# Performance work log

Measured on AMD Instinct MI355X. Metric: run time of the kernel, lower is better.

Reference implementation:

```python
import jax, jax.numpy as jnp
import numpy as np

N_NODES = 100000
LN_EPS = 1e-5
NEG_SLOPE = 0.2


def setup_inputs() -> dict:
    key = jax.random.key(0)
    ks = jax.random.split(key, 6)
    N, E, NIN, EDIM, NOUT, H = N_NODES, 1600000, 64, 32, 128, 4
    x = jax.random.normal(ks[0], (N, NIN), dtype=jnp.float32)
    edge_index = jax.random.randint(ks[1], (2, E), 0, N, dtype=jnp.int64)
    edge_attr = jax.random.normal(ks[2], (E, EDIM), dtype=jnp.float32)
    # xavier-uniform linear weights (torch layout: [out, in])
    def xavier(k, fan_out, fan_in):
        lim = float(np.sqrt(6.0 / (fan_in + fan_out)))
        return jax.random.uniform(k, (fan_out, fan_in), jnp.float32, -lim, lim)
    W_msg = xavier(ks[3], NOUT, NIN + EDIM)          # (128, 96)
    W_att = xavier(ks[4], H, 2 * NIN + EDIM)         # (4, 160)
    bias = jnp.zeros((NOUT,), jnp.float32)
    ln_gamma = jnp.ones((NOUT,), jnp.float32)
    ln_beta = jnp.zeros((NOUT,), jnp.float32)
    return {"x": x, "edge_index": edge_index, "edge_attr": edge_attr,
            "W_msg": W_msg, "W_att": W_att, "bias": bias,
            "ln_gamma": ln_gamma, "ln_beta": ln_beta}


def reference(x, edge_index, edge_attr, W_msg, W_att, bias, ln_gamma, ln_beta):
    N = x.shape[0]
    H = W_att.shape[0]
    src, dst = edge_index[0], edge_index[1]
    xs = x[src]                                       # (E, node_in) gather
    xd = x[dst]                                       # (E, node_in) gather
    # message: W_msg @ [h_u ; x_uv]
    msg_in = jnp.concatenate([xs, edge_attr], axis=-1)            # (E, 96)
    msgs = msg_in @ W_msg.T                                        # (E, out_dim)
    msgs = msgs.reshape(-1, H, W_msg.shape[0] // H)                # (E, H, D)
    # attention logits: LeakyReLU(W_att @ [h_u ; h_v ; x_uv])
    att_in = jnp.concatenate([xs, xd, edge_attr], axis=-1)         # (E, 160)
    logits = att_in @ W_att.T                                      # (E, H)
    logits = jax.nn.leaky_relu(logits, NEG_SLOPE)
    # per-destination-node sparse softmax
    seg_max = jax.ops.segment_max(logits, dst, num_segments=N)     # (N, H)
    exp_l = jnp.exp(logits - seg_max[dst])                         # (E, H)
    seg_sum = jax.ops.segment_sum(exp_l, dst, num_segments=N)      # (N, H)
    att = exp_l / (seg_sum[dst] + 1e-9)                            # (E, H)
    # weighted scatter-add aggregation
    weighted = msgs * att[..., None]                               # (E, H, D)
    out = jax.ops.segment_sum(weighted, dst, num_segments=N)       # (N, H, D)
    out = out.reshape(N, -1) + bias                                # concat heads
    # layer norm over feature dim
    mu = out.mean(axis=-1, keepdims=True)
    var = out.var(axis=-1, keepdims=True)
    out = (out - mu) * jax.lax.rsqrt(var + LN_EPS) * ln_gamma + ln_beta
    return out
```

## Files before the change

kernel.cpp:

```cpp
#include <hip/hip_runtime.h>
#include <hip/hip_bf16.h>

typedef __attribute__((ext_vector_type(8))) short short8;
typedef __attribute__((ext_vector_type(4))) float f32x4;

__device__ __forceinline__ unsigned short fbf(float f) {
  union { float f; unsigned u; } v; v.f = f;
  unsigned r = v.u + 0x7fffu + ((v.u >> 16) & 1u);
  return (unsigned short)(r >> 16);
}
__device__ __forceinline__ unsigned pk2(float a, float b) {
  return (unsigned)fbf(a) | ((unsigned)fbf(b) << 16);
}
__device__ __forceinline__ float ubf(unsigned hi) {
  union { unsigned u; float f; } v; v.u = hi << 16; return v.f;
}
__device__ __forceinline__ float ubf_lo(unsigned u) {
  union { unsigned u; float f; } v; v.u = u << 16; return v.f;
}
__device__ __forceinline__ float ubf_hi(unsigned u) {
  union { unsigned u; float f; } v; v.u = u & 0xffff0000u; return v.f;
}
__device__ __forceinline__ float dot4(float4 a, float4 b) {
  return fmaf(a.x, b.x, fmaf(a.y, b.y, fmaf(a.z, b.z, a.w * b.w)));
}

__launch_bounds__(256)
__global__ void k_phase1(const float* __restrict__ x, const float* __restrict__ W_att,
                         const int* __restrict__ edst, int E,
                         float4* __restrict__ A_s, float4* __restrict__ A_d,
                         unsigned* __restrict__ xb32, int* __restrict__ deg,
                         int* __restrict__ rank, int N) {
  __shared__ float4 s_wa[160];
  if (threadIdx.x < 160) s_wa[threadIdx.x] = ((const float4*)W_att)[threadIdx.x];
  for (int i = blockIdx.x * blockDim.x + threadIdx.x; i < E; i += gridDim.x * blockDim.x)
    rank[i] = atomicAdd(&deg[edst[i]], 1);
  __syncthreads();
  for (int v = blockIdx.x * blockDim.x + threadIdx.x; v < N; v += gridDim.x * blockDim.x) {
    const float4* xp = (const float4*)&x[v * 64];
    float4 xq[16];
    #pragma unroll
    for (int k = 0; k < 16; k++) xq[k] = xp[k];
    float as[4] = {}, ad[4] = {};
    #pragma unroll
    for (int h = 0; h < 4; h++) {
      #pragma unroll
      for (int k = 0; k < 16; k++) {
        as[h] += dot4(s_wa[h * 40 + k], xq[k]);
        ad[h] += dot4(s_wa[h * 40 + 16 + k], xq[k]);
      }
    }
    A_s[v] = make_float4(as[0], as[1], as[2], as[3]);
    A_d[v] = make_float4(ad[0], ad[1], ad[2], ad[3]);
    #pragma unroll
    for (int k = 0; k < 16; k++) {
      xb32[v * 32 + 2 * k]     = pk2(xq[k].x, xq[k].y);
      xb32[v * 32 + 2 * k + 1] = pk2(xq[k].z, xq[k].w);
    }
  }
}

__global__ void k_scan1(const int* __restrict__ deg, int N, int* __restrict__ part,
                        int* __restrict__ bsum) {
  __shared__ int tmp[1024];
  int tid = threadIdx.x;
  int i = blockIdx.x * 1024 + tid;
  int dv = (i < N) ? deg[i] : 0;
  int v = (dv + 7) & ~7;
  tmp[tid] = v;
  __syncthreads();
  for (int ofs = 1; ofs < 1024; ofs <<= 1) {
    int t = (tid >= ofs) ? tmp[tid - ofs] : 0;
    __syncthreads();
    tmp[tid] += t;
    __syncthreads();
  }
  if (i < N) part[i] = tmp[tid] - v;
  if (tid == 1023) bsum[blockIdx.x] = tmp[tid];
}

__global__ void k_scan2(int* __restrict__ part, const int* __restrict__ bsum,
                        const int* __restrict__ deg, int N, int4* __restrict__ csrp) {
  __shared__ int sbase;
  if (threadIdx.x == 0) {
    int b = 0;
    for (int j = 0; j < (int)blockIdx.x; j++) b += bsum[j];
    sbase = b;
  }
  __syncthreads();
  int i = blockIdx.x * 1024 + threadIdx.x;
  if (i < N) {
    const int o = part[i] + sbase;
    part[i] = o;
    const int d = deg[i];
    const int pe = o + ((d + 7) & ~7);
    const int4 z = make_int4(0, 0, 0, 0);
    for (int s = o + d; s < pe; s++) csrp[s] = z;
    if (i == N - 1) part[N] = pe;
  }
}

__launch_bounds__(256)
__global__ void k_att2(const int* __restrict__ esrc, const int* __restrict__ edst, int E,
                       const float* __restrict__ ea, const float4* __restrict__ A_s,
                       const float4* __restrict__ A_d, const float* __restrict__ W_att,
                       uint2* __restrict__ att_eo, unsigned short* __restrict__ eab) {
  __shared__ float4 s_we[32];
  if (threadIdx.x < 32) {
    int h = threadIdx.x >> 3, k4 = threadIdx.x & 7;
    const float* p = &W_att[h * 160 + 128 + k4 * 4];
    s_we[threadIdx.x] = make_float4(p[0], p[1], p[2], p[3]);
  }
  __syncthreads();
  for (int e = blockIdx.x * blockDim.x + threadIdx.x; e < E; e += gridDim.x * blockDim.x) {
    const int s = esrc[e], d = edst[e];
    const float4* ep = (const float4*)&ea[(unsigned)e * 32u];
    float4 eq[8];
    #pragma unroll
    for (int k = 0; k < 8; k++) eq[k] = ep[k];
    if (eab) {
      uint4* eo = (uint4*)(eab + (size_t)e * 32u);
      uint4 u;
      u.x = pk2(eq[0].x, eq[0].y); u.y = pk2(eq[0].z, eq[0].w);
      u.z = pk2(eq[1].x, eq[1].y); u.w = pk2(eq[1].z, eq[1].w);
      eo[0] = u;
      u.x = pk2(eq[2].x, eq[2].y); u.y = pk2(eq[2].z, eq[2].w);
      u.z = pk2(eq[3].x, eq[3].y); u.w = pk2(eq[3].z, eq[3].w);
      eo[1] = u;
      u.x = pk2(eq[4].x, eq[4].y); u.y = pk2(eq[4].z, eq[4].w);
      u.z = pk2(eq[5].x, eq[5].y); u.w = pk2(eq[5].z, eq[5].w);
      eo[2] = u;
      u.x = pk2(eq[6].x, eq[6].y); u.y = pk2(eq[6].z, eq[6].w);
      u.z = pk2(eq[7].x, eq[7].y); u.w = pk2(eq[7].z, eq[7].w);
      eo[3] = u;
    }
    const float4 as4 = A_s[s], ad4 = A_d[d];
    const float base[4] = {as4.x + ad4.x, as4.y + ad4.y, as4.z + ad4.z, as4.w + ad4.w};
    float av[4];
    #pragma unroll
    for (int h = 0; h < 4; h++) {
      float lg = base[h];
      #pragma unroll
      for (int k = 0; k < 8; k++) lg += dot4(s_we[h * 8 + k], eq[k]);
      lg = fmaxf(lg, 0.2f * lg);
      av[h] = __expf(lg);
    }
    att_eo[e] = make_uint2(pk2(av[0], av[1]), pk2(av[2], av[3]));
  }
}

__launch_bounds__(256)
__global__ void k_scat(const int* __restrict__ esrc, const int* __restrict__ edst,
                       const int* __restrict__ rank, const int* __restrict__ offsets,
                       const uint2* __restrict__ att_eo, int E, int4* __restrict__ csrp) {
  for (int e = blockIdx.x * blockDim.x + threadIdx.x; e < E; e += gridDim.x * blockDim.x) {
    const int d = edst[e];
    const int slot = offsets[d] + rank[e];
    const uint2 a = att_eo[e];
    csrp[slot] = make_int4(esrc[e], e, (int)a.x, (int)a.y);
  }
}

__launch_bounds__(256)
__global__ void k_aggP(const unsigned short* __restrict__ xb, const float* __restrict__ ea,
                       const int4* __restrict__ csrp, const int* __restrict__ offsets,
                       unsigned short* __restrict__ agg, float* __restrict__ denom, int N) {
  __shared__ int4 s_ids[4][2][32];
  const int lane = threadIdx.x & 63;
  const int wvb = threadIdx.x >> 6;
  const int wv = (blockIdx.x * blockDim.x + threadIdx.x) >> 6;
  const int nw = (gridDim.x * blockDim.x) >> 6;
  const int l32 = lane & 31;
  const bool hi = lane >= 32;

  if (wv >= N) return;
  int v0 = wv;
  int sstart = __builtin_amdgcn_readfirstlane(offsets[v0]);
  int send   = __builtin_amdgcn_readfirstlane(offsets[v0 + 1]);
  int4 pre = csrp[sstart + l32];
  int buf = 0;

  while (true) {
    const int ng = (send - sstart) >> 3;
    const int nq = (ng + 3) >> 2;
    const int vn = v0 + nw;
    const int vc = (vn < N) ? vn : (N - 1);
    const int sstart_n = __builtin_amdgcn_readfirstlane(offsets[vc]);
    const int send_n   = __builtin_amdgcn_readfirstlane(offsets[vc + 1]);

    float ax0 = 0, ax1 = 0, ax2 = 0, ax3 = 0;
    float ae0 = 0, ae1 = 0, ae2 = 0, ae3 = 0;
    float dn0 = 0, dn1 = 0, dn2 = 0, dn3 = 0;

    for (int q = 0; q < nq; q++) {
      if (lane < 32) s_ids[wvb][buf][l32] = pre;
      const int nbase = (q + 1 < nq) ? (sstart + (q + 1) * 32) : sstart_n;
      pre = csrp[nbase + l32];
      const int nsc = min(4, ng - q * 4);
      float ev[4][8];
      unsigned short qv[4][8];
      #pragma unroll
      for (int sc = 0; sc < 4; sc++) {
        if (sc < nsc) {
          #pragma unroll
          for (int p = 0; p < 8; p++) {
            const int4 t_ = s_ids[wvb][buf][sc * 8 + p];
            qv[sc][p] = xb[(unsigned)(t_.x << 6) + lane];
            ev[sc][p] = ea[(unsigned)(t_.y << 5) + l32];
          }
        }
      }
      #pragma unroll
      for (int sc = 0; sc < 4; sc++) {
        if (sc < nsc) {
          #pragma unroll
          for (int p = 0; p < 8; p++) {
            const int4 t_ = s_ids[wvb][buf][sc * 8 + p];
            const float a0_ = ubf_lo((unsigned)t_.z);
            const float a1_ = ubf_hi((unsigned)t_.z);
            const float a2_ = ubf_lo((unsigned)t_.w);
            const float a3_ = ubf_hi((unsigned)t_.w);
            const float xf = ubf((unsigned)qv[sc][p]);
            const float evp = ev[sc][p];
            ax0 = fmaf(a0_, xf, ax0); ax1 = fmaf(a1_, xf, ax1);
            ax2 = fmaf(a2_, xf, ax2); ax3 = fmaf(a3_, xf, ax3);
            ae0 = fmaf(a0_, evp, ae0); ae1 = fmaf(a1_, evp, ae1);
            ae2 = fmaf(a2_, evp, ae2); ae3 = fmaf(a3_, evp, ae3);
            dn0 += a0_; dn1 += a1_; dn2 += a2_; dn3 += a3_;
          }
        }
      }
      buf ^= 1;
    }
    if (nq == 0) pre = csrp[sstart_n + l32];

    const unsigned base = (unsigned)v0 * 384u;
    agg[base + lane]        = fbf(ax0);
    agg[base + 96 + lane]   = fbf(ax1);
    agg[base + 192 + lane]  = fbf(ax2);
    agg[base + 288 + lane]  = fbf(ax3);
    const int hA = hi ? 2 : 0;
    agg[base + hA * 96 + 64 + l32]       = fbf(hi ? ae2 : ae0);
    agg[base + (hA + 1) * 96 + 64 + l32] = fbf(hi ? ae3 : ae1);
    if (lane == 0) ((float4*)denom)[v0] = make_float4(dn0, dn1, dn2, dn3);

    if (vn >= N) break;
    v0 = vn; sstart = sstart_n; send = send_n;
  }
}

__launch_bounds__(256)
__global__ void k_aggPb(const unsigned short* __restrict__ xb,
                        const unsigned short* __restrict__ eab,
                        const int4* __restrict__ csrp, const int* __restrict__ offsets,
                        unsigned short* __restrict__ agg, float* __restrict__ denom, int N) {
  __shared__ int4 s_ids[4][2][32];
  const int lane = threadIdx.x & 63;
  const int wvb = threadIdx.x >> 6;
  const int wv = (blockIdx.x * blockDim.x + threadIdx.x) >> 6;
  const int nw = (gridDim.x * blockDim.x) >> 6;
  const int l32 = lane & 31;
  const bool hi = lane >= 32;

  if (wv >= N) return;
  int v0 = wv;
  int sstart = __builtin_amdgcn_readfirstlane(offsets[v0]);
  int send   = __builtin_amdgcn_readfirstlane(offsets[v0 + 1]);
  int4 pre = csrp[sstart + l32];
  int buf = 0;

  while (true) {
    const int ng = (send - sstart) >> 3;
    const int nq = (ng + 3) >> 2;
    const int vn = v0 + nw;
    const int vc = (vn < N) ? vn : (N - 1);
    const int sstart_n = __builtin_amdgcn_readfirstlane(offsets[vc]);
    const int send_n   = __builtin_amdgcn_readfirstlane(offsets[vc + 1]);

    float ax0 = 0, ax1 = 0, ax2 = 0, ax3 = 0;
    float ae0 = 0, ae1 = 0, ae2 = 0, ae3 = 0;
    float dn0 = 0, dn1 = 0, dn2 = 0, dn3 = 0;

    for (int q = 0; q < nq; q++) {
      if (lane < 32) s_ids[wvb][buf][l32] = pre;
      const int nbase = (q + 1 < nq) ? (sstart + (q + 1) * 32) : sstart_n;
      pre = csrp[nbase + l32];
      const int nsc = min(4, ng - q * 4);
      unsigned short evb[4][8];
      unsigned short qv[4][8];
      #pragma unroll
      for (int sc = 0; sc < 4; sc++) {
        if (sc < nsc) {
          #pragma unroll
          for (int p = 0; p < 8; p++) {
            const int4 t_ = s_ids[wvb][buf][sc * 8 + p];
            qv[sc][p] = xb[(unsigned)(t_.x << 6) + lane];
            evb[sc][p] = eab[(unsigned)(t_.y << 5) + l32];
          }
        }
      }
      #pragma unroll
      for (int sc = 0; sc < 4; sc++) {
        if (sc < nsc) {
          #pragma unroll
          for (int p = 0; p < 8; p++) {
            const int4 t_ = s_ids[wvb][buf][sc * 8 + p];
            const float a0_ = ubf_lo((unsigned)t_.z);
            const float a1_ = ubf_hi((unsigned)t_.z);
            const float a2_ = ubf_lo((unsigned)t_.w);
            const float a3_ = ubf_hi((unsigned)t_.w);
            const float xf = ubf((unsigned)qv[sc][p]);
            const float evp = ubf((unsigned)evb[sc][p]);
            ax0 = fmaf(a0_, xf, ax0); ax1 = fmaf(a1_, xf, ax1);
            ax2 = fmaf(a2_, xf, ax2); ax3 = fmaf(a3_, xf, ax3);
            ae0 = fmaf(a0_, evp, ae0); ae1 = fmaf(a1_, evp, ae1);
            ae2 = fmaf(a2_, evp, ae2); ae3 = fmaf(a3_, evp, ae3);
            dn0 += a0_; dn1 += a1_; dn2 += a2_; dn3 += a3_;
          }
        }
      }
      buf ^= 1;
    }
    if (nq == 0) pre = csrp[sstart_n + l32];

    const unsigned base = (unsigned)v0 * 384u;
    agg[base + lane]        = fbf(ax0);
    agg[base + 96 + lane]   = fbf(ax1);
    agg[base + 192 + lane]  = fbf(ax2);
    agg[base + 288 + lane]  = fbf(ax3);
    const int hA = hi ? 2 : 0;
    agg[base + hA * 96 + 64 + l32]       = fbf(hi ? ae2 : ae0);
    agg[base + (hA + 1) * 96 + 64 + l32] = fbf(hi ? ae3 : ae1);
    if (lane == 0) ((float4*)denom)[v0] = make_float4(dn0, dn1, dn2, dn3);

    if (vn >= N) break;
    v0 = vn; sstart = sstart_n; send = send_n;
  }
}

__launch_bounds__(128)
__global__ void k_out(const unsigned short* __restrict__ agg, const float* __restrict__ W_msg,
                      const float* __restrict__ denom, const float* __restrict__ bias,
                      const float* __restrict__ gamma, const float* __restrict__ beta,
                      float* __restrict__ out, int N, int T) {
  __shared__ float s_den[64];
  __shared__ float s_sum[2][16], s_sq[2][16];
  const int f = threadIdx.x;
  const int w = f >> 6;
  const int l = f & 63;
  const int c16 = l & 15;
  const int rg = l >> 4;

  short8 wb[2][2][3];
  float biasv[2][2], gv[2][2], bv[2][2];
  #pragma unroll
  for (int hh = 0; hh < 2; hh++) {
    const int head = 2 * w + hh;
    #pragma unroll
    for (int ct = 0; ct < 2; ct++) {
      const int q = head * 32 + ct * 16 + c16;
      biasv[hh][ct] = bias[q]; gv[hh][ct] = gamma[q]; bv[hh][ct] = beta[q];
      #pragma unroll
      for (int kk = 0; kk < 3; kk++) {
        const float* p = &W_msg[q * 96 + kk * 32 + rg * 8];
        short8 s;
        #pragma unroll
        for (int i = 0; i < 8; i++) s[i] = (short)fbf(p[i]);
        wb[hh][ct][kk] = s;
      }
    }
  }

  for (int t = blockIdx.x; t < T; t += gridDim.x) {
    const int n0 = t * 16;
    if (f < 64) s_den[f] = denom[min(n0 + (f >> 2), N - 1) * 4 + (f & 3)];
    __syncthreads();

    f32x4 c[2][2] = {{{0.f,0.f,0.f,0.f},{0.f,0.f,0.f,0.f}},
                     {{0.f,0.f,0.f,0.f},{0.f,0.f,0.f,0.f}}};
    const int nA = min(n0 + c16, N - 1);
    #pragma unroll
    for (int hh = 0; hh < 2; hh++) {
      const int head = 2 * w + hh;
      #pragma unroll
      for (int kk = 0; kk < 3; kk++) {
        short8 a = *(const short8*)&agg[nA * 384 + head * 96 + kk * 32 + rg * 8];
        c[hh][0] = __builtin_amdgcn_mfma_f32_16x16x32_bf16(a, wb[hh][0][kk], c[hh][0], 0, 0, 0);
        c[hh][1] = __builtin_amdgcn_mfma_f32_16x16x32_bf16(a, wb[hh][1][kk], c[hh][1], 0, 0, 0);
      }
    }

    float val[2][2][4];
    #pragma unroll
    for (int hh = 0; hh < 2; hh++)
      #pragma unroll
      for (int ct = 0; ct < 2; ct++)
        #pragma unroll
        for (int r = 0; r < 4; r++) {
          const float d = s_den[(rg * 4 + r) * 4 + (2 * w + hh)] + 1e-9f;
          val[hh][ct][r] = c[hh][ct][r] / d + biasv[hh][ct];
        }

    float sr[4], qr[4];
    #pragma unroll
    for (int r = 0; r < 4; r++) {
      float s = 0.f, q2 = 0.f;
      #pragma unroll
      for (int hh = 0; hh < 2; hh++)
        #pragma unroll
        for (int ct = 0; ct < 2; ct++) { s += val[hh][ct][r]; q2 = fmaf(val[hh][ct][r], val[hh][ct][r], q2); }
      #pragma unroll
      for (int m = 1; m <= 8; m <<= 1) { s += __shfl_xor(s, m, 64); q2 += __shfl_xor(q2, m, 64); }
      sr[r] = s; qr[r] = q2;
    }
    if (c16 == 0) {
      #pragma unroll
      for (int r = 0; r < 4; r++) { s_sum[w][rg * 4 + r] = sr[r]; s_sq[w][rg * 4 + r] = qr[r]; }
    }
    __syncthreads();

    float mean[4], rstd[4];
    #pragma unroll
    for (int r = 0; r < 4; r++) {
      const int ni = rg * 4 + r;
      mean[r] = (s_sum[0][ni] + s_sum[1][ni]) * (1.f / 128.f);
      const float m2 = (s_sq[0][ni] + s_sq[1][ni]) * (1.f / 128.f);
      rstd[r] = rsqrtf(m2 - mean[r] * mean[r] + 1e-5f);
    }
    #pragma unroll
    for (int hh = 0; hh < 2; hh++)
      #pragma unroll
      for (int ct = 0; ct < 2; ct++)
        #pragma unroll
        for (int r = 0; r < 4; r++) {
          const int n = n0 + rg * 4 + r;
          if (n < N)
            out[n * 128 + (2 * w + hh) * 32 + ct * 16 + c16] =
                (val[hh][ct][r] - mean[r]) * rstd[r] * gv[hh][ct] + bv[hh][ct];
        }
    __syncthreads();
  }
}

extern "C" void kernel_launch(void* const* d_in, const int* in_sizes, int n_in,
                              void* d_out, int out_size, void* d_ws, size_t ws_size,
                              hipStream_t stream) {
  const float* x     = (const float*)d_in[0];
  const int*   ei    = (const int*)d_in[1];
  const float* ea    = (const float*)d_in[2];
  const float* W_msg = (const float*)d_in[3];
  const float* W_att = (const float*)d_in[4];
  const float* bias  = (const float*)d_in[5];
  const float* gamma = (const float*)d_in[6];
  const float* beta  = (const float*)d_in[7];
  float* out = (float*)d_out;

  const int N = in_sizes[0] / 64;
  const int E = in_sizes[1] / 2;
  const int* esrc = ei;
  const int* edst = ei + E;
  const int EP = E + 8 * N + 64;

  char* p = (char*)d_ws;
  int* deg      = (int*)p;            p += (size_t)N * 4;
  int* offsets  = (int*)p;            p += (size_t)(N + 1) * 4;
  int* rank     = (int*)p;            p += (size_t)E * 4;
  int* bsum     = (int*)p;            p += 2048 * 4;
  int4* csrp    = (int4*)p;           p += (size_t)EP * 16;
  float4* A_s   = (float4*)p;         p += (size_t)N * 16;
  float4* A_d   = (float4*)p;         p += (size_t)N * 16;
  unsigned short* xb = (unsigned short*)p; p += (size_t)N * 64 * 2;
  unsigned short* agg = (unsigned short*)p; p += (size_t)N * 384 * 2;
  float* denom  = (float*)p;          p += (size_t)N * 16;
  uint2* att_eo = (uint2*)agg;
  unsigned short* eab = (unsigned short*)p; p += (size_t)E * 32 * 2;
  const bool use_eab = ((size_t)(p - (char*)d_ws) <= ws_size);

  hipMemsetAsync(deg, 0, (size_t)N * 4, stream);
  const int SB = (N + 1023) / 1024;
  const int T = (N + 15) / 16;

  k_phase1<<<4096, 256, 0, stream>>>(x, W_att, edst, E, A_s, A_d, (unsigned*)xb, deg, rank, N);
  k_scan1<<<SB, 1024, 0, stream>>>(deg, N, offsets, bsum);
  k_scan2<<<SB, 1024, 0, stream>>>(offsets, bsum, deg, N, csrp);
  k_att2<<<4096, 256, 0, stream>>>(esrc, edst, E, ea, A_s, A_d, W_att, att_eo,
                                   use_eab ? eab : (unsigned short*)nullptr);
  k_scat<<<4096, 256, 0, stream>>>(esrc, edst, rank, offsets, att_eo, E, csrp);
  if (use_eab)
    k_aggPb<<<4096, 256, 0, stream>>>(xb, eab, csrp, offsets, agg, denom, N);
  else
    k_aggP<<<4096, 256, 0, stream>>>(xb, ea, csrp, offsets, agg, denom, N);
  k_out<<<T, 128, 0, stream>>>(agg, W_msg, denom, bias, gamma, beta, out, N, T);
}
```

Baseline: 413.8 us.

## Cooperative 8-lane per-edge attention and split edge-attr gather across half-waves

The attention-logit kernel now assigns 8 lanes to each edge. Each lane loads one float4 of edge attributes, writes its bf16 copy and forms partial dot products that are reduced with xor shuffles. This replaces per-thread strided row reads with coalesced accesses. In the aggregation kernel, the two half-waves each gather edge attributes for alternating edges and combine their partial sums with a cross-half shuffle, halving the redundant eab loads. The new kernel writes eab without a null check, so it would fault if the workspace were too small.

```diff
diff --git a/kernel.cpp b/kernel.cpp
--- a/kernel.cpp
+++ b/kernel.cpp
@@ -101,51 +101,45 @@
 }
 
 __launch_bounds__(256)
-__global__ void k_att2(const int* __restrict__ esrc, const int* __restrict__ edst, int E,
+__global__ void k_att3(const int* __restrict__ esrc, const int* __restrict__ edst, int E,
                        const float* __restrict__ ea, const float4* __restrict__ A_s,
                        const float4* __restrict__ A_d, const float* __restrict__ W_att,
                        uint2* __restrict__ att_eo, unsigned short* __restrict__ eab) {
-  __shared__ float4 s_we[32];
-  if (threadIdx.x < 32) {
-    int h = threadIdx.x >> 3, k4 = threadIdx.x & 7;
-    const float* p = &W_att[h * 160 + 128 + k4 * 4];
-    s_we[threadIdx.x] = make_float4(p[0], p[1], p[2], p[3]);
-  }
-  __syncthreads();
-  for (int e = blockIdx.x * blockDim.x + threadIdx.x; e < E; e += gridDim.x * blockDim.x) {
-    const int s = esrc[e], d = edst[e];
-    const float4* ep = (const float4*)&ea[(unsigned)e * 32u];
-    float4 eq[8];
-    #pragma unroll
-    for (int k = 0; k < 8; k++) eq[k] = ep[k];
-    if (eab) {
-      uint4* eo = (uint4*)(eab + (size_t)e * 32u);
-      uint4 u;
-      u.x = pk2(eq[0].x, eq[0].y); u.y = pk2(eq[0].z, eq[0].w);
-      u.z = pk2(eq[1].x, eq[1].y); u.w = pk2(eq[1].z, eq[1].w);
-      eo[0] = u;
-      u.x = pk2(eq[2].x, eq[2].y); u.y = pk2(eq[2].z, eq[2].w);
-      u.z = pk2(eq[3].x, eq[3].y); u.w = pk2(eq[3].z, eq[3].w);
-      eo[1] = u;
-      u.x = pk2(eq[4].x, eq[4].y); u.y = pk2(eq[4].z, eq[4].w);
-      u.z = pk2(eq[5].x, eq[5].y); u.w = pk2(eq[5].z, eq[5].w);
-      eo[2] = u;
-      u.x = pk2(eq[6].x, eq[6].y); u.y = pk2(eq[6].z, eq[6].w);
-      u.z = pk2(eq[7].x, eq[7].y); u.w = pk2(eq[7].z, eq[7].w);
-      eo[3] = u;
-    }
-    const float4 as4 = A_s[s], ad4 = A_d[d];
-    const float base[4] = {as4.x + ad4.x, as4.y + ad4.y, as4.z + ad4.z, as4.w + ad4.w};
-    float av[4];
-    #pragma unroll
-    for (int h = 0; h < 4; h++) {
-      float lg = base[h];
-      #pragma unroll
-      for (int k = 0; k < 8; k++) lg += dot4(s_we[h * 8 + k], eq[k]);
-      lg = fmaxf(lg, 0.2f * lg);
-      av[h] = __expf(lg);
-    }
-    att_eo[e] = make_uint2(pk2(av[0], av[1]), pk2(av[2], av[3]));
+  const int lane = threadIdx.x & 63;
+  const int pj = lane >> 3;
+  const int jc = lane & 7;
+  const int wv = (blockIdx.x * blockDim.x + threadIdx.x) >> 6;
+  const int nw = (gridDim.x * blockDim.x) >> 6;
+
+  const float4 we0 = *(const float4*)&W_att[0 * 160 + 128 + jc * 4];
+  const float4 we1 = *(const float4*)&W_att[1 * 160 + 128 + jc * 4];
+  const float4 we2 = *(const float4*)&W_att[2 * 160 + 128 + jc * 4];
+  const float4 we3 = *(const float4*)&W_att[3 * 160 + 128 + jc * 4];
+
+  const int nE8 = (E + 7) >> 3;
+  for (int g = wv; g < nE8; g += nw) {
+    const int ereal = g * 8 + pj;
+    const int e = min(ereal, E - 1);
+    const float4 q = *(const float4*)&ea[(size_t)e * 32u + jc * 4];
+    *(uint2*)&eab[(size_t)e * 32u + jc * 4] =
+        make_uint2(pk2(q.x, q.y), pk2(q.z, q.w));
+    float lp0 = dot4(we0, q), lp1 = dot4(we1, q);
+    float lp2 = dot4(we2, q), lp3 = dot4(we3, q);
+    #pragma unroll
+    for (int m = 1; m <= 4; m <<= 1) {
+      lp0 += __shfl_xor(lp0, m, 64); lp1 += __shfl_xor(lp1, m, 64);
+      lp2 += __shfl_xor(lp2, m, 64); lp3 += __shfl_xor(lp3, m, 64);
+    }
+    if (jc == 0 && ereal < E) {
+      const int s = esrc[e], d = edst[e];
+      const float4 as4 = A_s[s], ad4 = A_d[d];
+      float lg0 = lp0 + as4.x + ad4.x; lg0 = fmaxf(lg0, 0.2f * lg0);
+      float lg1 = lp1 + as4.y + ad4.y; lg1 = fmaxf(lg1, 0.2f * lg1);
+      float lg2 = lp2 + as4.z + ad4.z; lg2 = fmaxf(lg2, 0.2f * lg2);
+      float lg3 = lp3 + as4.w + ad4.w; lg3 = fmaxf(lg3, 0.2f * lg3);
+      att_eo[e] = make_uint2(pk2(__expf(lg0), __expf(lg1)),
+                             pk2(__expf(lg2), __expf(lg3)));
+    }
   }
 }
 
@@ -261,6 +255,7 @@
   const int nw = (gridDim.x * blockDim.x) >> 6;
   const int l32 = lane & 31;
   const bool hi = lane >= 32;
+  const int hsel = hi ? 1 : 0;
 
   if (wv >= N) return;
   int v0 = wv;
@@ -286,7 +281,7 @@
       const int nbase = (q + 1 < nq) ? (sstart + (q + 1) * 32) : sstart_n;
       pre = csrp[nbase + l32];
       const int nsc = min(4, ng - q * 4);
-      unsigned short evb[4][8];
+      unsigned short evb[4][4];
       unsigned short qv[4][8];
       #pragma unroll
       for (int sc = 0; sc < 4; sc++) {
@@ -295,7 +290,11 @@
           for (int p = 0; p < 8; p++) {
             const int4 t_ = s_ids[wvb][buf][sc * 8 + p];
             qv[sc][p] = xb[(unsigned)(t_.x << 6) + lane];
-            evb[sc][p] = eab[(unsigned)(t_.y << 5) + l32];
+          }
+          #pragma unroll
+          for (int i = 0; i < 4; i++) {
+            const int4 te = s_ids[wvb][buf][sc * 8 + 2 * i + hsel];
+            evb[sc][i] = eab[(unsigned)(te.y << 5) + l32];
           }
         }
       }
@@ -310,18 +309,29 @@
             const float a2_ = ubf_lo((unsigned)t_.w);
             const float a3_ = ubf_hi((unsigned)t_.w);
             const float xf = ubf((unsigned)qv[sc][p]);
-            const float evp = ubf((unsigned)evb[sc][p]);
             ax0 = fmaf(a0_, xf, ax0); ax1 = fmaf(a1_, xf, ax1);
             ax2 = fmaf(a2_, xf, ax2); ax3 = fmaf(a3_, xf, ax3);
+            dn0 += a0_; dn1 += a1_; dn2 += a2_; dn3 += a3_;
+          }
+          #pragma unroll
+          for (int i = 0; i < 4; i++) {
+            const int4 te = s_ids[wvb][buf][sc * 8 + 2 * i + hsel];
+            const float a0_ = ubf_lo((unsigned)te.z);
+            const float a1_ = ubf_hi((unsigned)te.z);
+            const float a2_ = ubf_lo((unsigned)te.w);
+            const float a3_ = ubf_hi((unsigned)te.w);
+            const float evp = ubf((unsigned)evb[sc][i]);
             ae0 = fmaf(a0_, evp, ae0); ae1 = fmaf(a1_, evp, ae1);
             ae2 = fmaf(a2_, evp, ae2); ae3 = fmaf(a3_, evp, ae3);
-            dn0 += a0_; dn1 += a1_; dn2 += a2_; dn3 += a3_;
           }
         }
       }
       buf ^= 1;
     }
     if (nq == 0) pre = csrp[sstart_n + l32];
+
+    ae0 += __shfl_xor(ae0, 32, 64); ae1 += __shfl_xor(ae1, 32, 64);
+    ae2 += __shfl_xor(ae2, 32, 64); ae3 += __shfl_xor(ae3, 32, 64);
 
     const unsigned base = (unsigned)v0 * 384u;
     agg[base + lane]        = fbf(ax0);
@@ -483,7 +493,7 @@
   k_phase1<<<4096, 256, 0, stream>>>(x, W_att, edst, E, A_s, A_d, (unsigned*)xb, deg, rank, N);
   k_scan1<<<SB, 1024, 0, stream>>>(deg, N, offsets, bsum);
   k_scan2<<<SB, 1024, 0, stream>>>(offsets, bsum, deg, N, csrp);
-  k_att2<<<4096, 256, 0, stream>>>(esrc, edst, E, ea, A_s, A_d, W_att, att_eo,
+  k_att3<<<4096, 256, 0, stream>>>(esrc, edst, E, ea, A_s, A_d, W_att, att_eo,
                                    use_eab ? eab : (unsigned short*)nullptr);
   k_scat<<<4096, 256, 0, stream>>>(esrc, edst, rank, offsets, att_eo, E, csrp);
   if (use_eab)
```

Result: no change. 414.5 us (+0.2%).
